# Performance work log

Hardware: AMD Instinct MI355X
Metric: run time of the kernel (lower is better)

## Reference

```python
import jax, jax.numpy as jnp
import numpy as np

E, H, I, K, T = 32, 2048, 768, 4, 2048


def setup_inputs() -> dict:
    key = jax.random.key(0)
    k1, k2, k3, k4, k5 = jax.random.split(key, 5)
    hidden_states = jax.random.normal(k1, (T, H), dtype=jnp.float32)
    top_k_index = jax.random.randint(k2, (T, K), 0, E, dtype=jnp.int64)
    top_k_weights = jax.random.uniform(k3, (T, K), dtype=jnp.float32)
    gate_up_proj = jax.random.normal(k4, (E, H, 2 * I), dtype=jnp.float32) * 0.02
    down_proj = jax.random.normal(k5, (E, I, H), dtype=jnp.float32) * 0.02
    return {
        "hidden_states": hidden_states,
        "top_k_index": top_k_index,
        "top_k_weights": top_k_weights,
        "gate_up_proj": gate_up_proj,
        "down_proj": down_proj,
    }


def reference(hidden_states, top_k_index, top_k_weights, gate_up_proj, down_proj):
    # Dense routing-weight matrix [T, E]: zeros scattered with top-k weights
    num_tokens = hidden_states.shape[0]
    routing = jnp.zeros((num_tokens, E), dtype=hidden_states.dtype)
    routing = routing.at[jnp.arange(num_tokens)[:, None], top_k_index].set(top_k_weights)

    # Batched (grouped) GEMM over all experts; weights are stored transposed
    # gate_up_proj: [E, H, 2I] -> gu: [E, T, 2I]
    gu = jnp.einsum('th,ehi->eti', hidden_states, gate_up_proj)
    gate, up = jnp.split(gu, 2, axis=-1)           # each [E, T, I]
    inter = jax.nn.silu(gate) * up                 # [E, T, I]
    # down_proj: [E, I, H] -> per-expert output [E, T, H]
    expert_out = jnp.einsum('eti,eih->eth', inter, down_proj)
    # Weighted combine over experts
    out = jnp.einsum('te,eth->th', routing, expert_out)
    return out
```

## Files before the change

### kernel.cpp

```cpp
#include <hip/hip_runtime.h>
#include <hip/hip_bf16.h>

#define E_ 32
#define H_ 2048
#define I_ 768
#define K_ 4
#define T_ 2048
#define TWO_I 1536
#define MAXT 8

typedef __attribute__((ext_vector_type(8))) short short8;
typedef __attribute__((ext_vector_type(4))) float floatx4;

#define WS_OFFSETS 0
#define WS_IDS     1024
#define WS_WTS     (1024 + 32768)
#define WS_INTER   131072

__device__ __forceinline__ unsigned short f2bf(float f) {
  union { float f; unsigned u; } v; v.f = f;
  unsigned r = v.u + 0x7FFFu + ((v.u >> 16) & 1u);
  return (unsigned short)(r >> 16);
}

__device__ __forceinline__ short8 cvt8(float4 a, float4 b) {
  short8 r;
  r[0] = (short)f2bf(a.x); r[1] = (short)f2bf(a.y);
  r[2] = (short)f2bf(a.z); r[3] = (short)f2bf(a.w);
  r[4] = (short)f2bf(b.x); r[5] = (short)f2bf(b.y);
  r[6] = (short)f2bf(b.z); r[7] = (short)f2bf(b.w);
  return r;
}

__global__ void build_routing(const int* __restrict__ idx, const float* __restrict__ w,
                              char* __restrict__ ws) {
  int* offs = (int*)(ws + WS_OFFSETS);
  int* ids  = (int*)(ws + WS_IDS);
  float* wt = (float*)(ws + WS_WTS);
  __shared__ int s_cnt[E_];
  __shared__ int s_pos[E_];
  int tid = threadIdx.x;
  if (tid < E_) s_cnt[tid] = 0;
  __syncthreads();
  for (int i = tid; i < T_ * K_; i += 256) {
    int t = i >> 2, j = i & 3;
    int e = idx[i];
    bool keep = true;
    for (int j2 = j + 1; j2 < K_; ++j2) if (idx[t * K_ + j2] == e) keep = false;
    if (keep) atomicAdd(&s_cnt[e], 1);
  }
  __syncthreads();
  if (tid == 0) {
    int run = 0;
    for (int e = 0; e < E_; ++e) { offs[e] = run; s_pos[e] = run; run += s_cnt[e]; }
    offs[E_] = run;
  }
  __syncthreads();
  for (int i = tid; i < T_ * K_; i += 256) {
    int t = i >> 2, j = i & 3;
    int e = idx[i];
    bool keep = true;
    for (int j2 = j + 1; j2 < K_; ++j2) if (idx[t * K_ + j2] == e) keep = false;
    if (keep) {
      int p = atomicAdd(&s_pos[e], 1);
      ids[p] = t;
      wt[p] = w[i];
    }
  }
}

__global__ __launch_bounds__(256, 2) void gemm1(
    const float* __restrict__ hidden, const float* __restrict__ gup,
    char* __restrict__ ws) {
  const int* offs = (const int*)(ws + WS_OFFSETS);
  const int* ids  = (const int*)(ws + WS_IDS);
  unsigned short* inter = (unsigned short*)(ws + WS_INTER);

  int e = blockIdx.x, mt = blockIdx.y, nt = blockIdx.z;
  int start = offs[e];
  int cnt = offs[e + 1] - start;
  int m0 = mt * 128;
  if (m0 >= cnt) return;
  int mrem = cnt - m0;
  int n0 = nt * 64;

  __shared__ __align__(16) unsigned short Al[128][40];
  __shared__ __align__(16) unsigned short Bl[128][40];

  int tid = threadIdx.x;
  int lane = tid & 63, wid = tid >> 6;
  int wy = wid >> 1, wx = wid & 1;
  int quad = lane >> 4, l15 = lane & 15;

  floatx4 acc[4][4];
#pragma unroll
  for (int a = 0; a < 4; ++a)
#pragma unroll
    for (int b = 0; b < 4; ++b) acc[a][b] = (floatx4){0.f, 0.f, 0.f, 0.f};

  int am[2], ak[2], tok[2];
#pragma unroll
  for (int u = 0; u < 2; ++u) {
    int lin = tid + u * 256;
    am[u] = lin >> 2; ak[u] = (lin & 3) * 8;
    tok[u] = (am[u] < mrem) ? ids[start + m0 + am[u]] : -1;
  }
  int bj = tid & 127;
  int bk0 = (tid >> 7) * 16;
  int gc = (bj < 64) ? (n0 + bj) : (I_ + n0 + (bj - 64));
  const float* gbase = gup + (size_t)e * H_ * TWO_I + gc;

  for (int kb = 0; kb < H_ / 32; ++kb) {
#pragma unroll
    for (int u = 0; u < 2; ++u) {
      short8 av = (short8){0, 0, 0, 0, 0, 0, 0, 0};
      if (tok[u] >= 0) {
        const float* src = hidden + tok[u] * H_ + kb * 32 + ak[u];
        av = cvt8(*(const float4*)src, *(const float4*)(src + 4));
      }
      *(short8*)&Al[am[u]][ak[u]] = av;
    }
    {
      const float* gk = gbase + (size_t)(kb * 32 + bk0) * TWO_I;
      unsigned short bv[16];
#pragma unroll
      for (int kr = 0; kr < 16; ++kr) bv[kr] = f2bf(gk[(size_t)kr * TWO_I]);
      short8 b0, b1;
#pragma unroll
      for (int q = 0; q < 8; ++q) { b0[q] = (short)bv[q]; b1[q] = (short)bv[8 + q]; }
      *(short8*)&Bl[bj][bk0] = b0;
      *(short8*)&Bl[bj][bk0 + 8] = b1;
    }
    __syncthreads();

    short8 af[4], bfr[4];
#pragma unroll
    for (int mi = 0; mi < 4; ++mi)
      af[mi] = *(const short8*)&Al[wy * 64 + mi * 16 + l15][quad * 8];
#pragma unroll
    for (int ni = 0; ni < 4; ++ni) {
      int j = (ni < 2) ? (wx * 32 + ni * 16 + l15) : (64 + wx * 32 + (ni - 2) * 16 + l15);
      bfr[ni] = *(const short8*)&Bl[j][quad * 8];
    }
#pragma unroll
    for (int mi = 0; mi < 4; ++mi)
#pragma unroll
      for (int ni = 0; ni < 4; ++ni)
        acc[mi][ni] = __builtin_amdgcn_mfma_f32_16x16x32_bf16(af[mi], bfr[ni], acc[mi][ni], 0, 0, 0);
    __syncthreads();
  }

#pragma unroll
  for (int mi = 0; mi < 4; ++mi) {
#pragma unroll
    for (int r = 0; r < 4; ++r) {
      int row = wy * 64 + mi * 16 + quad * 4 + r;
      if (row < mrem) {
        int slot = start + m0 + row;
#pragma unroll
        for (int ni = 0; ni < 2; ++ni) {
          float g = acc[mi][ni][r];
          float u = acc[mi][ni + 2][r];
          float s = g / (1.f + __expf(-g));
          int col = n0 + wx * 32 + ni * 16 + l15;
          inter[(size_t)slot * I_ + col] = f2bf(s * u);
        }
      }
    }
  }
}

__global__ __launch_bounds__(256, 2) void gemm2(
    const float* __restrict__ down, float* __restrict__ out, char* __restrict__ ws) {
  const int* offs = (const int*)(ws + WS_OFFSETS);
  const int* ids  = (const int*)(ws + WS_IDS);
  const float* wt = (const float*)(ws + WS_WTS);
  const unsigned short* inter = (const unsigned short*)(ws + WS_INTER);

  int e = blockIdx.x, mt = blockIdx.y, nt = blockIdx.z;
  int start = offs[e];
  int cnt = offs[e + 1] - start;
  int m0 = mt * 128;
  if (m0 >= cnt) return;
  int mrem = cnt - m0;
  int n0 = nt * 128;

  __shared__ __align__(16) unsigned short Al[128][40];
  __shared__ __align__(16) unsigned short Bl[128][40];

  int tid = threadIdx.x;
  int lane = tid & 63, wid = tid >> 6;
  int wy = wid >> 1, wx = wid & 1;
  int quad = lane >> 4, l15 = lane & 15;

  floatx4 acc[4][4];
#pragma unroll
  for (int a = 0; a < 4; ++a)
#pragma unroll
    for (int b = 0; b < 4; ++b) acc[a][b] = (floatx4){0.f, 0.f, 0.f, 0.f};

  int am[2], ak[2];
#pragma unroll
  for (int u = 0; u < 2; ++u) {
    int lin = tid + u * 256;
    am[u] = lin >> 2; ak[u] = (lin & 3) * 8;
  }
  int bj = tid & 127;
  int bk0 = (tid >> 7) * 16;
  const float* dbase = down + (size_t)e * I_ * H_ + (n0 + bj);

  for (int kb = 0; kb < I_ / 32; ++kb) {
#pragma unroll
    for (int u = 0; u < 2; ++u) {
      uint4 av = (uint4){0u, 0u, 0u, 0u};
      if (am[u] < mrem)
        av = *(const uint4*)(inter + (size_t)(start + m0 + am[u]) * I_ + kb * 32 + ak[u]);
      *(uint4*)&Al[am[u]][ak[u]] = av;
    }
    {
      const float* dk = dbase + (size_t)(kb * 32 + bk0) * H_;
      unsigned short bv[16];
#pragma unroll
      for (int kr = 0; kr < 16; ++kr) bv[kr] = f2bf(dk[(size_t)kr * H_]);
      short8 b0, b1;
#pragma unroll
      for (int q = 0; q < 8; ++q) { b0[q] = (short)bv[q]; b1[q] = (short)bv[8 + q]; }
      *(short8*)&Bl[bj][bk0] = b0;
      *(short8*)&Bl[bj][bk0 + 8] = b1;
    }
    __syncthreads();

    short8 af[4], bfr[4];
#pragma unroll
    for (int mi = 0; mi < 4; ++mi)
      af[mi] = *(const short8*)&Al[wy * 64 + mi * 16 + l15][quad * 8];
#pragma unroll
    for (int ni = 0; ni < 4; ++ni)
      bfr[ni] = *(const short8*)&Bl[wx * 64 + ni * 16 + l15][quad * 8];
#pragma unroll
    for (int mi = 0; mi < 4; ++mi)
#pragma unroll
      for (int ni = 0; ni < 4; ++ni)
        acc[mi][ni] = __builtin_amdgcn_mfma_f32_16x16x32_bf16(af[mi], bfr[ni], acc[mi][ni], 0, 0, 0);
    __syncthreads();
  }

#pragma unroll
  for (int mi = 0; mi < 4; ++mi) {
#pragma unroll
    for (int r = 0; r < 4; ++r) {
      int row = wy * 64 + mi * 16 + quad * 4 + r;
      if (row < mrem) {
        int slot = start + m0 + row;
        int t = ids[slot];
        float w = wt[slot];
#pragma unroll
        for (int ni = 0; ni < 4; ++ni) {
          int col = n0 + wx * 64 + ni * 16 + l15;
          atomicAdd(out + (size_t)t * H_ + col, w * acc[mi][ni][r]);
        }
      }
    }
  }
}

extern "C" void kernel_launch(void* const* d_in, const int* in_sizes, int n_in,
                              void* d_out, int out_size, void* d_ws, size_t ws_size,
                              hipStream_t stream) {
  (void)in_sizes; (void)n_in; (void)out_size; (void)ws_size;
  const float* hidden = (const float*)d_in[0];
  const int* idx      = (const int*)d_in[1];
  const float* w      = (const float*)d_in[2];
  const float* gup    = (const float*)d_in[3];
  const float* down   = (const float*)d_in[4];
  float* out = (float*)d_out;
  char* ws = (char*)d_ws;

  hipMemsetAsync(d_out, 0, (size_t)T_ * H_ * sizeof(float), stream);
  build_routing<<<1, 256, 0, stream>>>(idx, w, ws);
  gemm1<<<dim3(E_, MAXT, I_ / 64), 256, 0, stream>>>(hidden, gup, ws);
  gemm2<<<dim3(E_, MAXT, H_ / 128), 256, 0, stream>>>(down, out, ws);
}
```

Measured before the change: 923.6 us.

## Compact tile list, pre-convert hidden to bf16, and register-prefetch K=64 tiles

Routing now emits a compact list of (expert, m-tile) pairs, so the GEMM grids launch only real tiles instead of a mostly-empty E×MAXT grid. A new kernel converts hidden states to bf16 once, which removes the repeated fp32 loads and conversions in gemm1. Both GEMMs move to a K-step of 64 and prefetch the next tile's global loads into registers while the current tile computes, and they use the packed bf16 conversion intrinsic. In exchange, register pressure rises because 32 fp32 B values are held per thread, shared memory per block grows, and the conversion adds an extra launch and workspace traffic.

```diff
diff --git a/kernel.cpp b/kernel.cpp
--- a/kernel.cpp
+++ b/kernel.cpp
@@ -4,10 +4,9 @@
 #define E_ 32
 #define H_ 2048
 #define I_ 768
-#define K_ 4
 #define T_ 2048
 #define TWO_I 1536
-#define MAXT 8
+#define MAX_TILES 96
 
 typedef __attribute__((ext_vector_type(8))) short short8;
 typedef __attribute__((ext_vector_type(4))) float floatx4;
@@ -15,7 +14,9 @@
 #define WS_OFFSETS 0
 #define WS_IDS     1024
 #define WS_WTS     (1024 + 32768)
+#define WS_TILES   (1024 + 65536)
 #define WS_INTER   131072
+#define WS_HID16   (131072 + 8192*768*2)
 
 __device__ __forceinline__ unsigned short f2bf(float f) {
   union { float f; unsigned u; } v; v.f = f;
@@ -23,13 +24,9 @@
   return (unsigned short)(r >> 16);
 }
 
-__device__ __forceinline__ short8 cvt8(float4 a, float4 b) {
-  short8 r;
-  r[0] = (short)f2bf(a.x); r[1] = (short)f2bf(a.y);
-  r[2] = (short)f2bf(a.z); r[3] = (short)f2bf(a.w);
-  r[4] = (short)f2bf(b.x); r[5] = (short)f2bf(b.y);
-  r[6] = (short)f2bf(b.z); r[7] = (short)f2bf(b.w);
-  return r;
+__device__ __forceinline__ unsigned pkbf(float a, float b) {
+  __hip_bfloat162 h = __float22bfloat162_rn(float2{a, b});
+  union { __hip_bfloat162 h; unsigned u; } v; v.h = h; return v.u;
 }
 
 __global__ void build_routing(const int* __restrict__ idx, const float* __restrict__ w,
@@ -37,16 +34,17 @@
   int* offs = (int*)(ws + WS_OFFSETS);
   int* ids  = (int*)(ws + WS_IDS);
   float* wt = (float*)(ws + WS_WTS);
+  int* tiles = (int*)(ws + WS_TILES);
   __shared__ int s_cnt[E_];
   __shared__ int s_pos[E_];
   int tid = threadIdx.x;
   if (tid < E_) s_cnt[tid] = 0;
   __syncthreads();
-  for (int i = tid; i < T_ * K_; i += 256) {
+  for (int i = tid; i < T_ * 4; i += 256) {
     int t = i >> 2, j = i & 3;
     int e = idx[i];
     bool keep = true;
-    for (int j2 = j + 1; j2 < K_; ++j2) if (idx[t * K_ + j2] == e) keep = false;
+    for (int j2 = j + 1; j2 < 4; ++j2) if (idx[t * 4 + j2] == e) keep = false;
     if (keep) atomicAdd(&s_cnt[e], 1);
   }
   __syncthreads();
@@ -54,13 +52,17 @@
     int run = 0;
     for (int e = 0; e < E_; ++e) { offs[e] = run; s_pos[e] = run; run += s_cnt[e]; }
     offs[E_] = run;
+    int nt = 0;
+    for (int e = 0; e < E_; ++e)
+      for (int m0 = 0; m0 < s_cnt[e]; m0 += 128) tiles[nt++] = (e << 16) | (m0 >> 7);
+    for (; nt < MAX_TILES; ++nt) tiles[nt] = -1;
   }
   __syncthreads();
-  for (int i = tid; i < T_ * K_; i += 256) {
+  for (int i = tid; i < T_ * 4; i += 256) {
     int t = i >> 2, j = i & 3;
     int e = idx[i];
     bool keep = true;
-    for (int j2 = j + 1; j2 < K_; ++j2) if (idx[t * K_ + j2] == e) keep = false;
+    for (int j2 = j + 1; j2 < 4; ++j2) if (idx[t * 4 + j2] == e) keep = false;
     if (keep) {
       int p = atomicAdd(&s_pos[e], 1);
       ids[p] = t;
@@ -69,84 +71,99 @@
   }
 }
 
+__global__ void cvt_hidden(const float* __restrict__ hs, char* __restrict__ ws) {
+  int g = blockIdx.x * 256 + threadIdx.x;
+  const float4 f0 = ((const float4*)hs)[g * 2];
+  const float4 f1 = ((const float4*)hs)[g * 2 + 1];
+  uint4 o;
+  o.x = pkbf(f0.x, f0.y); o.y = pkbf(f0.z, f0.w);
+  o.z = pkbf(f1.x, f1.y); o.w = pkbf(f1.z, f1.w);
+  ((uint4*)(ws + WS_HID16))[g] = o;
+}
+
 __global__ __launch_bounds__(256, 2) void gemm1(
-    const float* __restrict__ hidden, const float* __restrict__ gup,
-    char* __restrict__ ws) {
+    const float* __restrict__ gup, char* __restrict__ ws) {
   const int* offs = (const int*)(ws + WS_OFFSETS);
   const int* ids  = (const int*)(ws + WS_IDS);
+  const int* tiles = (const int*)(ws + WS_TILES);
+  const unsigned short* h16 = (const unsigned short*)(ws + WS_HID16);
   unsigned short* inter = (unsigned short*)(ws + WS_INTER);
 
-  int e = blockIdx.x, mt = blockIdx.y, nt = blockIdx.z;
+  int tl = tiles[blockIdx.y];
+  if (tl < 0) return;
+  int e = tl >> 16, m0 = (tl & 0xffff) << 7;
   int start = offs[e];
-  int cnt = offs[e + 1] - start;
-  int m0 = mt * 128;
-  if (m0 >= cnt) return;
-  int mrem = cnt - m0;
-  int n0 = nt * 64;
-
-  __shared__ __align__(16) unsigned short Al[128][40];
-  __shared__ __align__(16) unsigned short Bl[128][40];
-
-  int tid = threadIdx.x;
-  int lane = tid & 63, wid = tid >> 6;
-  int wy = wid >> 1, wx = wid & 1;
-  int quad = lane >> 4, l15 = lane & 15;
-
-  floatx4 acc[4][4];
-#pragma unroll
-  for (int a = 0; a < 4; ++a)
-#pragma unroll
-    for (int b = 0; b < 4; ++b) acc[a][b] = (floatx4){0.f, 0.f, 0.f, 0.f};
-
-  int am[2], ak[2], tok[2];
-#pragma unroll
-  for (int u = 0; u < 2; ++u) {
+  int mrem = offs[e + 1] - start - m0;
+  int n0 = blockIdx.x * 64;
+
+  __shared__ __align__(16) unsigned short Al[128][72];
+  __shared__ __align__(16) unsigned short Bl[128][72];
+
+  int tid = threadIdx.x, lane = tid & 63, wid = tid >> 6;
+  int wy = wid >> 1, wx = wid & 1, quad = lane >> 4, l15 = lane & 15;
+
+  floatx4 acc[4][4] = {};
+
+  int arow[4], ako[4];
+  const unsigned short* asrc[4];
+#pragma unroll
+  for (int u = 0; u < 4; ++u) {
     int lin = tid + u * 256;
-    am[u] = lin >> 2; ak[u] = (lin & 3) * 8;
-    tok[u] = (am[u] < mrem) ? ids[start + m0 + am[u]] : -1;
+    arow[u] = lin >> 3; ako[u] = (lin & 7) * 8;
+    int tok = (arow[u] < mrem) ? ids[start + m0 + arow[u]] : -1;
+    asrc[u] = (tok >= 0) ? h16 + (size_t)tok * H_ + ako[u] : nullptr;
   }
   int bj = tid & 127;
-  int bk0 = (tid >> 7) * 16;
+  int kr0 = (tid >> 7) * 32;
   int gc = (bj < 64) ? (n0 + bj) : (I_ + n0 + (bj - 64));
   const float* gbase = gup + (size_t)e * H_ * TWO_I + gc;
 
-  for (int kb = 0; kb < H_ / 32; ++kb) {
-#pragma unroll
-    for (int u = 0; u < 2; ++u) {
-      short8 av = (short8){0, 0, 0, 0, 0, 0, 0, 0};
-      if (tok[u] >= 0) {
-        const float* src = hidden + tok[u] * H_ + kb * 32 + ak[u];
-        av = cvt8(*(const float4*)src, *(const float4*)(src + 4));
+  uint4 pf_a[4];
+  float pf_b[32];
+
+  auto loadA = [&](int kb) {
+#pragma unroll
+    for (int u = 0; u < 4; ++u)
+      pf_a[u] = asrc[u] ? *(const uint4*)(asrc[u] + (size_t)kb * 64) : uint4{0u, 0u, 0u, 0u};
+  };
+  auto loadB = [&](int kb) {
+    const float* p = gbase + (size_t)(kb * 64 + kr0) * TWO_I;
+#pragma unroll
+    for (int r = 0; r < 32; ++r) pf_b[r] = p[(size_t)r * TWO_I];
+  };
+
+  loadA(0); loadB(0);
+  for (int kb = 0; kb < H_ / 64; ++kb) {
+#pragma unroll
+    for (int u = 0; u < 4; ++u) *(uint4*)&Al[arow[u]][ako[u]] = pf_a[u];
+#pragma unroll
+    for (int q = 0; q < 4; ++q) {
+      uint4 wv;
+      wv.x = pkbf(pf_b[q * 8 + 0], pf_b[q * 8 + 1]);
+      wv.y = pkbf(pf_b[q * 8 + 2], pf_b[q * 8 + 3]);
+      wv.z = pkbf(pf_b[q * 8 + 4], pf_b[q * 8 + 5]);
+      wv.w = pkbf(pf_b[q * 8 + 6], pf_b[q * 8 + 7]);
+      *(uint4*)&Bl[bj][kr0 + q * 8] = wv;
+    }
+    __syncthreads();
+    if (kb + 1 < H_ / 64) { loadA(kb + 1); loadB(kb + 1); }
+#pragma unroll
+    for (int ks = 0; ks < 2; ++ks) {
+      short8 af[4], bfr[4];
+#pragma unroll
+      for (int mi = 0; mi < 4; ++mi)
+        af[mi] = *(const short8*)&Al[wy * 64 + mi * 16 + l15][ks * 32 + quad * 8];
+#pragma unroll
+      for (int ni = 0; ni < 4; ++ni) {
+        int j = (ni < 2) ? (wx * 32 + ni * 16 + l15) : (64 + wx * 32 + (ni - 2) * 16 + l15);
+        bfr[ni] = *(const short8*)&Bl[j][ks * 32 + quad * 8];
       }
-      *(short8*)&Al[am[u]][ak[u]] = av;
-    }
-    {
-      const float* gk = gbase + (size_t)(kb * 32 + bk0) * TWO_I;
-      unsigned short bv[16];
-#pragma unroll
-      for (int kr = 0; kr < 16; ++kr) bv[kr] = f2bf(gk[(size_t)kr * TWO_I]);
-      short8 b0, b1;
-#pragma unroll
-      for (int q = 0; q < 8; ++q) { b0[q] = (short)bv[q]; b1[q] = (short)bv[8 + q]; }
-      *(short8*)&Bl[bj][bk0] = b0;
-      *(short8*)&Bl[bj][bk0 + 8] = b1;
-    }
-    __syncthreads();
-
-    short8 af[4], bfr[4];
-#pragma unroll
-    for (int mi = 0; mi < 4; ++mi)
-      af[mi] = *(const short8*)&Al[wy * 64 + mi * 16 + l15][quad * 8];
-#pragma unroll
-    for (int ni = 0; ni < 4; ++ni) {
-      int j = (ni < 2) ? (wx * 32 + ni * 16 + l15) : (64 + wx * 32 + (ni - 2) * 16 + l15);
-      bfr[ni] = *(const short8*)&Bl[j][quad * 8];
-    }
-#pragma unroll
-    for (int mi = 0; mi < 4; ++mi)
-#pragma unroll
-      for (int ni = 0; ni < 4; ++ni)
-        acc[mi][ni] = __builtin_amdgcn_mfma_f32_16x16x32_bf16(af[mi], bfr[ni], acc[mi][ni], 0, 0, 0);
+#pragma unroll
+      for (int mi = 0; mi < 4; ++mi)
+#pragma unroll
+        for (int ni = 0; ni < 4; ++ni)
+          acc[mi][ni] = __builtin_amdgcn_mfma_f32_16x16x32_bf16(af[mi], bfr[ni], acc[mi][ni], 0, 0, 0);
+    }
     __syncthreads();
   }
 
@@ -175,73 +192,80 @@
   const int* offs = (const int*)(ws + WS_OFFSETS);
   const int* ids  = (const int*)(ws + WS_IDS);
   const float* wt = (const float*)(ws + WS_WTS);
+  const int* tiles = (const int*)(ws + WS_TILES);
   const unsigned short* inter = (const unsigned short*)(ws + WS_INTER);
 
-  int e = blockIdx.x, mt = blockIdx.y, nt = blockIdx.z;
+  int tl = tiles[blockIdx.y];
+  if (tl < 0) return;
+  int e = tl >> 16, m0 = (tl & 0xffff) << 7;
   int start = offs[e];
-  int cnt = offs[e + 1] - start;
-  int m0 = mt * 128;
-  if (m0 >= cnt) return;
-  int mrem = cnt - m0;
-  int n0 = nt * 128;
-
-  __shared__ __align__(16) unsigned short Al[128][40];
-  __shared__ __align__(16) unsigned short Bl[128][40];
-
-  int tid = threadIdx.x;
-  int lane = tid & 63, wid = tid >> 6;
-  int wy = wid >> 1, wx = wid & 1;
-  int quad = lane >> 4, l15 = lane & 15;
-
-  floatx4 acc[4][4];
-#pragma unroll
-  for (int a = 0; a < 4; ++a)
-#pragma unroll
-    for (int b = 0; b < 4; ++b) acc[a][b] = (floatx4){0.f, 0.f, 0.f, 0.f};
-
-  int am[2], ak[2];
-#pragma unroll
-  for (int u = 0; u < 2; ++u) {
+  int mrem = offs[e + 1] - start - m0;
+  int n0 = blockIdx.x * 128;
+
+  __shared__ __align__(16) unsigned short Al[128][72];
+  __shared__ __align__(16) unsigned short Bl[128][72];
+
+  int tid = threadIdx.x, lane = tid & 63, wid = tid >> 6;
+  int wy = wid >> 1, wx = wid & 1, quad = lane >> 4, l15 = lane & 15;
+
+  floatx4 acc[4][4] = {};
+
+  int arow[4], ako[4];
+  const unsigned short* asrc[4];
+#pragma unroll
+  for (int u = 0; u < 4; ++u) {
     int lin = tid + u * 256;
-    am[u] = lin >> 2; ak[u] = (lin & 3) * 8;
+    arow[u] = lin >> 3; ako[u] = (lin & 7) * 8;
+    asrc[u] = (arow[u] < mrem) ? inter + (size_t)(start + m0 + arow[u]) * I_ + ako[u] : nullptr;
   }
   int bj = tid & 127;
-  int bk0 = (tid >> 7) * 16;
+  int kr0 = (tid >> 7) * 32;
   const float* dbase = down + (size_t)e * I_ * H_ + (n0 + bj);
 
-  for (int kb = 0; kb < I_ / 32; ++kb) {
-#pragma unroll
-    for (int u = 0; u < 2; ++u) {
-      uint4 av = (uint4){0u, 0u, 0u, 0u};
-      if (am[u] < mrem)
-        av = *(const uint4*)(inter + (size_t)(start + m0 + am[u]) * I_ + kb * 32 + ak[u]);
-      *(uint4*)&Al[am[u]][ak[u]] = av;
-    }
-    {
-      const float* dk = dbase + (size_t)(kb * 32 + bk0) * H_;
-      unsigned short bv[16];
-#pragma unroll
-      for (int kr = 0; kr < 16; ++kr) bv[kr] = f2bf(dk[(size_t)kr * H_]);
-      short8 b0, b1;
-#pragma unroll
-      for (int q = 0; q < 8; ++q) { b0[q] = (short)bv[q]; b1[q] = (short)bv[8 + q]; }
-      *(short8*)&Bl[bj][bk0] = b0;
-      *(short8*)&Bl[bj][bk0 + 8] = b1;
+  uint4 pf_a[4];
+  float pf_b[32];
+
+  auto loadA = [&](int kb) {
+#pragma unroll
+    for (int u = 0; u < 4; ++u)
+      pf_a[u] = asrc[u] ? *(const uint4*)(asrc[u] + (size_t)kb * 64) : uint4{0u, 0u, 0u, 0u};
+  };
+  auto loadB = [&](int kb) {
+    const float* p = dbase + (size_t)(kb * 64 + kr0) * H_;
+#pragma unroll
+    for (int r = 0; r < 32; ++r) pf_b[r] = p[(size_t)r * H_];
+  };
+
+  loadA(0); loadB(0);
+  for (int kb = 0; kb < I_ / 64; ++kb) {
+#pragma unroll
+    for (int u = 0; u < 4; ++u) *(uint4*)&Al[arow[u]][ako[u]] = pf_a[u];
+#pragma unroll
+    for (int q = 0; q < 4; ++q) {
+      uint4 wv;
+      wv.x = pkbf(pf_b[q * 8 + 0], pf_b[q * 8 + 1]);
+      wv.y = pkbf(pf_b[q * 8 + 2], pf_b[q * 8 + 3]);
+      wv.z = pkbf(pf_b[q * 8 + 4], pf_b[q * 8 + 5]);
+      wv.w = pkbf(pf_b[q * 8 + 6], pf_b[q * 8 + 7]);
+      *(uint4*)&Bl[bj][kr0 + q * 8] = wv;
     }
     __syncthreads();
-
-    short8 af[4], bfr[4];
-#pragma unroll
-    for (int mi = 0; mi < 4; ++mi)
-      af[mi] = *(const short8*)&Al[wy * 64 + mi * 16 + l15][quad * 8];
-#pragma unroll
-    for (int ni = 0; ni < 4; ++ni)
-      bfr[ni] = *(const short8*)&Bl[wx * 64 + ni * 16 + l15][quad * 8];
-#pragma unroll
-    for (int mi = 0; mi < 4; ++mi)
+    if (kb + 1 < I_ / 64) { loadA(kb + 1); loadB(kb + 1); }
+#pragma unroll
+    for (int ks = 0; ks < 2; ++ks) {
+      short8 af[4], bfr[4];
+#pragma unroll
+      for (int mi = 0; mi < 4; ++mi)
+        af[mi] = *(const short8*)&Al[wy * 64 + mi * 16 + l15][ks * 32 + quad * 8];
 #pragma unroll
       for (int ni = 0; ni < 4; ++ni)
-        acc[mi][ni] = __builtin_amdgcn_mfma_f32_16x16x32_bf16(af[mi], bfr[ni], acc[mi][ni], 0, 0, 0);
+        bfr[ni] = *(const short8*)&Bl[wx * 64 + ni * 16 + l15][ks * 32 + quad * 8];
+#pragma unroll
+      for (int mi = 0; mi < 4; ++mi)
+#pragma unroll
+        for (int ni = 0; ni < 4; ++ni)
+          acc[mi][ni] = __builtin_amdgcn_mfma_f32_16x16x32_bf16(af[mi], bfr[ni], acc[mi][ni], 0, 0, 0);
+    }
     __syncthreads();
   }
 
@@ -278,6 +302,7 @@
 
   hipMemsetAsync(d_out, 0, (size_t)T_ * H_ * sizeof(float), stream);
   build_routing<<<1, 256, 0, stream>>>(idx, w, ws);
-  gemm1<<<dim3(E_, MAXT, I_ / 64), 256, 0, stream>>>(hidden, gup, ws);
-  gemm2<<<dim3(E_, MAXT, H_ / 128), 256, 0, stream>>>(down, out, ws);
-}
+  cvt_hidden<<<T_ * H_ / 8 / 256, 256, 0, stream>>>(hidden, ws);
+  gemm1<<<dim3(I_ / 64, MAX_TILES), 256, 0, stream>>>(gup, ws);
+  gemm2<<<dim3(H_ / 128, MAX_TILES), 256, 0, stream>>>(down, out, ws);
+}
```

After: 821.0 us. 1.12x faster.
